# Performance work log

Measured on AMD Instinct MI355X. Metric: run time of the kernel, lower is better.

The kernel has to match this reference:

```python
import jax, jax.numpy as jnp
import numpy as np

B, N, C = 4, 4096, 512
K = 683  # ceil(N / ratio=6.0)
TAU = 1.0
W_OCC, W_REP, W_ENT = 1.0, 0.1, 0.01
REP_TOPK, REP_MARGIN = 4, -1.0
NEG = -1e9


def setup_inputs() -> dict:
    key = jax.random.key(0)
    ks = jax.random.split(key, 5)
    s = jax.random.normal(ks[0], (B, N, C), jnp.float32)
    mu = jax.random.normal(ks[1], (B, N, 3), jnp.float32)
    # SPD covariance per residue: L L^T + 0.1 I
    L = jax.random.normal(ks[2], (B, N, 3, 3), jnp.float32) * 0.3
    Sigma = jnp.einsum('bnij,bnkj->bnik', L, L) + 0.1 * jnp.eye(3, dtype=jnp.float32)
    mask = jnp.ones((B, N), jnp.float32)
    W = jax.random.normal(ks[3], (C, C), jnp.float32) / np.sqrt(C).astype(np.float32)
    b = jnp.zeros((C,), jnp.float32)
    slots = jax.random.normal(ks[4], (K, C), jnp.float32) * 0.02
    return {"s": s, "mu": mu, "Sigma": Sigma, "mask": mask, "W": W, "b": b, "slots": slots}


def reference(s, mu, Sigma, mask, W, b, slots):
    Kk = slots.shape[0]
    # A = softmax((Linear(s)) . slots / tau), masked
    s_proj = jnp.einsum('bnc,dc->bnd', s, W) + b            # nn.Linear: x @ W^T + b
    logits = jnp.einsum('bnc,kc->bnk', s_proj, slots) / TAU
    logits = jnp.where((mask < 0.5)[..., None], NEG, logits)
    A = jax.nn.softmax(logits, axis=-1) * mask[..., None]   # [B,N,K]

    denom = jnp.maximum(A.sum(axis=1), 1e-8)                # [B,K]
    s_c = jnp.einsum('bnk,bnc->bkc', A, s) / denom[..., None]

    # moment-matching merge
    w = A / (A.sum(axis=1, keepdims=True) + 1e-8)           # [B,N,K]
    mu_c = jnp.einsum('bnk,bnd->bkd', w, mu)                # [B,K,3]
    intra = jnp.einsum('bnk,bnij->bkij', w, Sigma)          # [B,K,3,3]
    diff = mu[:, :, None, :] - mu_c[:, None, :, :]          # [B,N,K,3]
    inter = jnp.einsum('bnk,bnki,bnkj->bkij', w, diff, diff)
    Sigma_c = intra + inter                                 # [B,K,3,3]

    # occupancy balance loss
    occ = A.sum(axis=1)
    occ = occ / jnp.maximum(occ.sum(axis=-1, keepdims=True), 1e-8)
    loss_occ = jnp.mean((occ - 1.0 / Kk) ** 2)

    # repulsion loss (pairwise Gaussian overlap)
    delta = mu_c[:, :, None, :] - mu_c[:, None, :, :]       # [B,K,K,3]
    sig_sum = Sigma_c[:, :, None] + Sigma_c[:, None, :]     # [B,K,K,3,3]
    inv = jnp.linalg.inv(sig_sum + 1e-6 * jnp.eye(3, dtype=s.dtype))
    dist2 = jnp.einsum('bpqi,bpqij,bpqj->bpq', delta, inv, delta)
    score = -0.5 * dist2
    eye = jnp.eye(Kk, dtype=bool)[None]
    score = jnp.where(eye, NEG, score)
    top = jax.lax.top_k(score, min(REP_TOPK, Kk - 1))[0]
    loss_rep = jnp.mean(jax.nn.relu(top - REP_MARGIN))

    # entropy loss
    Ac = jnp.maximum(A, 1e-8)
    ent = -(Ac * jnp.log(Ac)).sum(axis=-1)                  # [B,N]
    loss_ent = (ent * mask).sum() / jnp.maximum(mask.sum(), 1.0)

    total = W_OCC * loss_occ + W_REP * loss_rep + W_ENT * loss_ent
    return (A, s_c, mu_c, Sigma_c, loss_occ, loss_rep, loss_ent, total)
```

## Files before the change

kernel.cpp:

```cpp
#include <hip/hip_runtime.h>
#include <math.h>

#define B_    4
#define N_    4096
#define C_    512
#define KSLOT 683

using bf16x8 = __attribute__((ext_vector_type(8))) short;
using f32x4  = __attribute__((ext_vector_type(4))) float;

#define OFF_A    0
#define OFF_SC   (B_*N_*KSLOT)
#define OFF_MU   (OFF_SC + B_*KSLOT*C_)
#define OFF_SIG  (OFF_MU + B_*KSLOT*3)
#define OFF_LOSS (OFF_SIG + B_*KSLOT*9)

#define WS_MOM    0
#define WS_INVMAX (WS_MOM + B_*KSLOT*16)
#define WS_OCCTB  (WS_INVMAX + B_*KSLOT)
#define WS_OCCT   (WS_OCCTB + 256)
#define WS_ENTB   (WS_OCCT + 4)
#define WS_MSB    (WS_ENTB + 256)
#define WS_OCCLB  (WS_MSB + 256)
#define WS_REPB   (WS_OCCLB + 256)
#define WS_BS     (WS_REPB + 256)
#define WS_FEND   (WS_BS + 704)

#define US_BASE  (WS_FEND*2)
#define US_SBF   US_BASE
#define US_STF   (US_SBF + B_*N_*C_)
#define US_WSL   (US_STF + B_*C_*N_)
#define US_FT    (US_WSL + 704*C_)
#define US_ATB   (US_FT + B_*16*N_)
#define US_END   (US_ATB + (size_t)B_*768*N_)


__device__ __forceinline__ ushort f2bf(float x) {
  union { float f; unsigned u; } v; v.f = x;
  unsigned r = v.u + 0x7fffu + ((v.u >> 16) & 1u);
  return (ushort)(r >> 16);
}

__device__ __forceinline__ float blockSum256(float v, float* red) {
#pragma unroll
  for (int off = 32; off; off >>= 1) v += __shfl_xor(v, off);
  __syncthreads();
  if ((threadIdx.x & 63) == 0) red[threadIdx.x >> 6] = v;
  __syncthreads();
  return red[0] + red[1] + red[2] + red[3];
}

__device__ __forceinline__ void top4_insert(float v, float& t0, float& t1, float& t2, float& t3) {
  if (v > t3) {
    if (v > t2) {
      t3 = t2;
      if (v > t1) {
        t2 = t1;
        if (v > t0) { t1 = t0; t0 = v; } else t1 = v;
      } else t2 = v;
    } else t3 = v;
  }
}

__global__ __launch_bounds__(256) void prep_all(const float* __restrict__ s,
                                                ushort* __restrict__ sbf,
                                                ushort* __restrict__ stf,
                                                const float* __restrict__ mu,
                                                const float* __restrict__ Sig,
                                                ushort* __restrict__ ftg,
                                                const float* __restrict__ slots,
                                                const float* __restrict__ W,
                                                ushort* __restrict__ wsl,
                                                const float* __restrict__ bvec,
                                                float* __restrict__ bs) {
  __shared__ __align__(16) char PS[16640];
  const int bid = blockIdx.x;
  const int t = threadIdx.x;
  if (bid < 342) {
    float (*SL)[512] = (float(*)[512])PS;
    const int idx = bid;
    const int k0 = (idx % 171) * 4;
    const int c = (idx / 171) * 256 + t;
    for (int id2 = t; id2 < 4 * 512; id2 += 256) {
      int kk = id2 >> 9, d = id2 & 511;
      SL[kk][d] = (k0 + kk < KSLOT) ? slots[(size_t)(k0 + kk) * C_ + d] : 0.f;
    }
    __syncthreads();
    float acc[4];
#pragma unroll
    for (int i = 0; i < 4; ++i) acc[i] = 0.f;
    for (int d0 = 0; d0 < C_; d0 += 8) {
      float wv[8];
#pragma unroll
      for (int j = 0; j < 8; ++j) wv[j] = W[(size_t)(d0 + j) * C_ + c];
#pragma unroll
      for (int j = 0; j < 8; ++j) {
#pragma unroll
        for (int i = 0; i < 4; ++i) acc[i] += SL[i][d0 + j] * wv[j];
      }
    }
#pragma unroll
    for (int i = 0; i < 4; ++i)
      if (k0 + i < KSLOT) wsl[(size_t)(k0 + i) * C_ + c] = f2bf(acc[i]);
  } else if (bid < 513) {
    const int widx = (bid - 342) * 4 + (t >> 6);
    const int lane = t & 63;
    if (widx < KSLOT) {
      const float* srow = slots + (size_t)widx * C_;
      float acc = 0.f;
#pragma unroll
      for (int j = 0; j < 8; ++j) {
        int d = lane + j * 64;
        acc += srow[d] * bvec[d];
      }
#pragma unroll
      for (int off = 32; off; off >>= 1) acc += __shfl_xor(acc, off);
      if (lane == 0) bs[widx] = acc;
    }
  } else if (bid < 577) {
    ushort (*FT)[272] = (ushort(*)[272])PS;
    const int fb = bid - 513;
    const size_t ng = (size_t)fb * 256 + t;
    const float* mp = mu + ng * 3;
    const float* sp = Sig + ng * 9;
    float m0 = mp[0], m1 = mp[1], m2 = mp[2];
    FT[0][t] = 0x3F80;
    FT[1][t] = f2bf(m0); FT[2][t] = f2bf(m1); FT[3][t] = f2bf(m2);
    FT[4][t] = f2bf(m0 * m0); FT[5][t] = f2bf(m0 * m1); FT[6][t] = f2bf(m0 * m2);
    FT[7][t] = f2bf(m1 * m1); FT[8][t] = f2bf(m1 * m2); FT[9][t] = f2bf(m2 * m2);
    FT[10][t] = f2bf(sp[0]); FT[11][t] = f2bf(sp[1]); FT[12][t] = f2bf(sp[2]);
    FT[13][t] = f2bf(sp[4]); FT[14][t] = f2bf(sp[5]); FT[15][t] = f2bf(sp[8]);
    __syncthreads();
    const int b = (int)((fb * 256) >> 12);
    const int n0b = (fb * 256) & (N_ - 1);
    for (int u = t; u < 512; u += 256) {
      int f = u >> 5, off = (u & 31) * 8;
      *(uint4*)(ftg + ((size_t)b * 16 + f) * N_ + n0b + off) = *(uint4*)(&FT[f][off]);
    }
  } else {
    float (*T)[65] = (float(*)[65])PS;
    const int cid = bid - 577;
    const int b = cid >> 9;
    const int rem = cid & 511;
    const int n0 = (rem >> 3) * 64;
    const int c0 = (rem & 7) * 64;
    const int tr = t >> 4;
    const int tc = (t & 15) * 4;
#pragma unroll
    for (int i = 0; i < 4; ++i) {
      const int row = i * 16 + tr;
      float4 v = *(const float4*)(s + ((size_t)(b * N_ + n0 + row)) * C_ + c0 + tc);
      ushort4 u;
      u.x = f2bf(v.x); u.y = f2bf(v.y); u.z = f2bf(v.z); u.w = f2bf(v.w);
      *(ushort4*)(sbf + ((size_t)(b * N_ + n0 + row)) * C_ + c0 + tc) = u;
      T[row][tc + 0] = v.x; T[row][tc + 1] = v.y;
      T[row][tc + 2] = v.z; T[row][tc + 3] = v.w;
    }
    __syncthreads();
#pragma unroll
    for (int i = 0; i < 4; ++i) {
      const int c = i * 16 + tr;
      const int n4 = tc;
      ushort4 o;
      o.x = f2bf(T[n4 + 0][c]); o.y = f2bf(T[n4 + 1][c]);
      o.z = f2bf(T[n4 + 2][c]); o.w = f2bf(T[n4 + 3][c]);
      *(ushort4*)(stf + ((size_t)(b * C_ + c0 + c)) * N_ + n0 + n4) = o;
    }
  }
}

__global__ __launch_bounds__(256) void bs_kernel(const float* __restrict__ slots,
                                                 const float* __restrict__ bvec,
                                                 float* __restrict__ bs) {
  int k = blockIdx.x * 256 + threadIdx.x;
  if (k >= KSLOT) return;
  const float* srow = slots + (size_t)k * C_;
  float acc = 0.f;
  for (int d = 0; d < C_; ++d) acc += srow[d] * bvec[d];
  bs[k] = acc;
}

__device__ __forceinline__ void g1_epilogue(
    f32x4 (&acc)[11], const int rowbase, const int t, const int lane,
    const int rowg, const int colw,
    const float* __restrict__ bs, const float* __restrict__ mask,
    float* __restrict__ Aout, ushort* __restrict__ atb,
    float* __restrict__ entb, float* __restrict__ msb,
    float* Af, float (&red4)[32][4], const int binid) {
  __syncthreads();
  int cols[11]; bool valid[11];
#pragma unroll
  for (int cf = 0; cf < 11; ++cf) {
    cols[cf] = colw * 176 + cf * 16 + (lane & 15);
    valid[cf] = (cols[cf] < KSLOT);
    float bv = valid[cf] ? bs[cols[cf]] : 0.f;
#pragma unroll
    for (int r = 0; r < 4; ++r) acc[cf][r] += bv;
  }
  float m4[4];
#pragma unroll
  for (int r = 0; r < 4; ++r) m4[r] = -3.0e38f;
#pragma unroll
  for (int cf = 0; cf < 11; ++cf)
    if (valid[cf]) {
#pragma unroll
      for (int r = 0; r < 4; ++r) m4[r] = fmaxf(m4[r], acc[cf][r]);
    }
#pragma unroll
  for (int off = 1; off < 16; off <<= 1) {
#pragma unroll
    for (int r = 0; r < 4; ++r) m4[r] = fmaxf(m4[r], __shfl_xor(m4[r], off));
  }
  if ((lane & 15) == 0) {
#pragma unroll
    for (int r = 0; r < 4; ++r) red4[rowg * 16 + (lane >> 4) * 4 + r][colw] = m4[r];
  }
  __syncthreads();
#pragma unroll
  for (int r = 0; r < 4; ++r) {
    int rl = rowg * 16 + (lane >> 4) * 4 + r;
    m4[r] = fmaxf(fmaxf(red4[rl][0], red4[rl][1]), fmaxf(red4[rl][2], red4[rl][3]));
  }
  __syncthreads();
  float s4[4] = {0.f, 0.f, 0.f, 0.f};
#pragma unroll
  for (int cf = 0; cf < 11; ++cf)
    if (valid[cf]) {
#pragma unroll
      for (int r = 0; r < 4; ++r) {
        float e = __expf(acc[cf][r] - m4[r]);
        acc[cf][r] = e;
        s4[r] += e;
      }
    }
#pragma unroll
  for (int off = 1; off < 16; off <<= 1) {
#pragma unroll
    for (int r = 0; r < 4; ++r) s4[r] += __shfl_xor(s4[r], off);
  }
  if ((lane & 15) == 0) {
#pragma unroll
    for (int r = 0; r < 4; ++r) red4[rowg * 16 + (lane >> 4) * 4 + r][colw] = s4[r];
  }
  __syncthreads();
  float inv4[4], mr4[4];
#pragma unroll
  for (int r = 0; r < 4; ++r) {
    int rl = rowg * 16 + (lane >> 4) * 4 + r;
    float S = red4[rl][0] + red4[rl][1] + red4[rl][2] + red4[rl][3];
    inv4[r] = 1.f / S;
    mr4[r] = mask[rowbase + rl];
  }
  __syncthreads();
  float ent4[4] = {0.f, 0.f, 0.f, 0.f};
#pragma unroll
  for (int cf = 0; cf < 11; ++cf)
    if (valid[cf]) {
#pragma unroll
      for (int r = 0; r < 4; ++r) {
        int rl = rowg * 16 + (lane >> 4) * 4 + r;
        float a = acc[cf][r] * inv4[r] * mr4[r];
        Af[rl * KSLOT + cols[cf]] = a;
        float ac = fmaxf(a, 1e-8f);
        ent4[r] -= ac * __logf(ac);
      }
    }
#pragma unroll
  for (int off = 1; off < 16; off <<= 1) {
#pragma unroll
    for (int r = 0; r < 4; ++r) ent4[r] += __shfl_xor(ent4[r], off);
  }
  if ((lane & 15) == 0) {
#pragma unroll
    for (int r = 0; r < 4; ++r) red4[rowg * 16 + (lane >> 4) * 4 + r][colw] = ent4[r];
  }
  __syncthreads();
  if (t < 64) {
    float er = 0.f, ms = 0.f;
    if (t < 32) {
      float e = red4[t][0] + red4[t][1] + red4[t][2] + red4[t][3];
      float m = mask[rowbase + t];
      er = e * m; ms = m;
    }
#pragma unroll
    for (int off = 32; off; off >>= 1) { er += __shfl_xor(er, off); ms += __shfl_xor(ms, off); }
    if (t == 0) {
      atomicAdd(&entb[binid], er);
      atomicAdd(&msb[binid], ms);
    }
  }
  const float4* Af4 = (const float4*)Af;
  float4* Ag4 = (float4*)(Aout + (size_t)rowbase * KSLOT);
  for (int i = t; i < (32 * KSLOT) / 4; i += 512) Ag4[i] = Af4[i];
  {
    const int bb = rowbase >> 12;
    const int n0b = rowbase & (N_ - 1);
    ushort* Atb = atb + ((size_t)bb * 768) * N_ + n0b;
    for (int u = t; u < KSLOT * 4; u += 512) {
      int k = u >> 2, q = u & 3;
      ushort tmp[8];
#pragma unroll
      for (int j = 0; j < 8; ++j) tmp[j] = f2bf(Af[(q * 8 + j) * KSLOT + k]);
      *(uint4*)(Atb + (size_t)k * N_ + q * 8) = *(uint4*)tmp;
    }
  }
}

__global__ __launch_bounds__(512)
__attribute__((amdgpu_waves_per_eu(2, 2)))
void gemm1sm(const ushort* __restrict__ sbf,
             const ushort* __restrict__ wsl,
             const float* __restrict__ bs,
             const float* __restrict__ mask,
             float* __restrict__ Aout,
             ushort* __restrict__ atb,
             float* __restrict__ entb,
             float* __restrict__ msb) {
  __shared__ __align__(16) char SMEM[90112];
  float* Af = (float*)SMEM;
  __shared__ float red4[32][4];
  const int t = threadIdx.x;
  const int lane = t & 63;
  const int w = t >> 6;
  const int rowg = w >> 2;
  const int colw = w & 3;
  const int row0 = blockIdx.x * 64;
  const int r16 = rowg * 16 + (lane & 15);

  const ushort* arow0 = sbf + (size_t)(row0 + r16) * C_ + (lane >> 4) * 8;
  const ushort* arow1 = arow0 + (size_t)32 * C_;
  bf16x8 g0a = *(const bf16x8*)(arow0);
  bf16x8 g0b = *(const bf16x8*)(arow0 + 32);
  bf16x8 g1a = *(const bf16x8*)(arow1);
  bf16x8 g1b = *(const bf16x8*)(arow1 + 32);
  bf16x8 p0a, p0b, p1a, p1b;

  f32x4 acc0[11], acc1[11];
  f32x4 zero = {0.f, 0.f, 0.f, 0.f};
#pragma unroll
  for (int cf = 0; cf < 11; ++cf) { acc0[cf] = zero; acc1[cf] = zero; }

#pragma unroll
  for (int slab = 0; slab < 8; ++slab) {
    if (slab) __syncthreads();
#pragma unroll
    for (int i = 0; i < 11; ++i) {
      int idx = t + i * 512;
      int r = idx >> 3;
      int chs = (idx & 7) ^ (r & 7);
      const ushort* g = wsl + (size_t)r * C_ + slab * 64 + chs * 8;
      char* l = (char*)SMEM + i * 8192 + (t & 448) * 16;
      __builtin_amdgcn_global_load_lds(
          (const __attribute__((address_space(1))) void*)g,
          (__attribute__((address_space(3))) void*)l, 16, 0, 0);
    }
    __syncthreads();
    if (slab < 7) {
      p0a = *(const bf16x8*)(arow0 + (slab + 1) * 64);
      p0b = *(const bf16x8*)(arow0 + (slab + 1) * 64 + 32);
      p1a = *(const bf16x8*)(arow1 + (slab + 1) * 64);
      p1b = *(const bf16x8*)(arow1 + (slab + 1) * 64 + 32);
    }
    {
      const int ach0 = (lane >> 4);
#pragma unroll
      for (int cf = 0; cf < 11; ++cf) {
        int br = colw * 176 + cf * 16 + (lane & 15);
        bf16x8 bf = *(const bf16x8*)(SMEM + br * 128 + ((ach0 * 16) ^ ((br & 7) << 4)));
        acc0[cf] = __builtin_amdgcn_mfma_f32_16x16x32_bf16(g0a, bf, acc0[cf], 0, 0, 0);
        acc1[cf] = __builtin_amdgcn_mfma_f32_16x16x32_bf16(g1a, bf, acc1[cf], 0, 0, 0);
      }
      const int ach1 = 4 + (lane >> 4);
#pragma unroll
      for (int cf = 0; cf < 11; ++cf) {
        int br = colw * 176 + cf * 16 + (lane & 15);
        bf16x8 bf = *(const bf16x8*)(SMEM + br * 128 + ((ach1 * 16) ^ ((br & 7) << 4)));
        acc0[cf] = __builtin_amdgcn_mfma_f32_16x16x32_bf16(g0b, bf, acc0[cf], 0, 0, 0);
        acc1[cf] = __builtin_amdgcn_mfma_f32_16x16x32_bf16(g1b, bf, acc1[cf], 0, 0, 0);
      }
    }
    g0a = p0a; g0b = p0b; g1a = p1a; g1b = p1b;
  }

  g1_epilogue(acc0, row0, t, lane, rowg, colw, bs, mask, Aout, atb, entb, msb,
              Af, red4, (blockIdx.x * 2) & 255);
  g1_epilogue(acc1, row0 + 32, t, lane, rowg, colw, bs, mask, Aout, atb, entb, msb,
              Af, red4, (blockIdx.x * 2 + 1) & 255);
}

#define G2BUFB 18432
__global__ __launch_bounds__(256) void gemm2t(const ushort* __restrict__ atb,
                                              const ushort* __restrict__ stf,
                                              const ushort* __restrict__ ftg,
                                              float* __restrict__ sc,
                                              float* __restrict__ MOM) {
  __shared__ __align__(16) char LB[2 * G2BUFB];
  const int t = threadIdx.x;
  const int lane = t & 63;
  const int w = t >> 6;
  const int wm = w >> 1;
  const int wn = w & 1;
  const int fhw = blockIdx.x;
  const int logical = (fhw & 7) * 44 + (fhw >> 3);
  const int kt = logical % 11;
  const int ct = (logical / 11) & 7;
  const int b  = logical / 88;
  const bool do_mom = (ct == 0);
  const ushort* Ab = atb + ((size_t)b * 768 + kt * 64) * N_;
  const ushort* Sb = stf + ((size_t)b * C_ + ct * 64) * N_;
  const ushort* Fb = ftg + ((size_t)b * 16) * N_;

  f32x4 zero = {0.f, 0.f, 0.f, 0.f};
  f32x4 acc[2][2];
#pragma unroll
  for (int i = 0; i < 2; ++i)
#pragma unroll
    for (int j = 0; j < 2; ++j) acc[i][j] = zero;
  f32x4 accf[2];
#pragma unroll
  for (int i = 0; i < 2; ++i) accf[i] = zero;

#define G2_STAGE(BUFI, NB)                                                   \
  {                                                                          \
    char* AtL = LB + (BUFI) * G2BUFB;                                        \
    char* SsL = AtL + 8192;                                                  \
    char* FtL = AtL + 16384;                                                 \
    _Pragma("unroll")                                                        \
    for (int i = 0; i < 2; ++i) {                                            \
      int idx = t + i * 256;                                                 \
      int r = idx >> 3;                                                      \
      int chs = (idx & 7) ^ (r & 7);                                         \
      const ushort* g = Ab + (size_t)r * N_ + (NB) + chs * 8;                \
      char* l = AtL + i * 4096 + (t & 192) * 16;                             \
      __builtin_amdgcn_global_load_lds(                                      \
          (const __attribute__((address_space(1))) void*)g,                  \
          (__attribute__((address_space(3))) void*)l, 16, 0, 0);             \
    }                                                                        \
    _Pragma("unroll")                                                        \
    for (int i = 0; i < 2; ++i) {                                            \
      int idx = t + i * 256;                                                 \
      int r = idx >> 3;                                                      \
      int chs = (idx & 7) ^ (r & 7);                                         \
      const ushort* g = Sb + (size_t)r * N_ + (NB) + chs * 8;                \
      char* l = SsL + i * 4096 + (t & 192) * 16;                             \
      __builtin_amdgcn_global_load_lds(                                      \
          (const __attribute__((address_space(1))) void*)g,                  \
          (__attribute__((address_space(3))) void*)l, 16, 0, 0);             \
    }                                                                        \
    if (do_mom && t < 128) {                                                 \
      int idx = t;                                                           \
      int r = idx >> 3;                                                      \
      int chs = (idx & 7) ^ (r & 7);                                         \
      const ushort* g = Fb + (size_t)r * N_ + (NB) + chs * 8;                \
      char* l = FtL + (t & 192) * 16;                                        \
      __builtin_amdgcn_global_load_lds(                                      \
          (const __attribute__((address_space(1))) void*)g,                  \
          (__attribute__((address_space(3))) void*)l, 16, 0, 0);             \
    }                                                                        \
  }

  G2_STAGE(0, 0)
  for (int st = 0; st < 64; ++st) {
    const int cur = st & 1;
    __syncthreads();
    if (st < 63) G2_STAGE(cur ^ 1, (st + 1) * 64)
    char* AtL = LB + cur * G2BUFB;
    char* SsL = AtL + 8192;
    char* FtL = AtL + 16384;
#pragma unroll
    for (int ks2 = 0; ks2 < 2; ++ks2) {
      const int ach = ks2 * 4 + (lane >> 4);
      bf16x8 afr[2], bfr[2];
#pragma unroll
      for (int kf = 0; kf < 2; ++kf) {
        int ar = wm * 32 + kf * 16 + (lane & 15);
        afr[kf] = *(const bf16x8*)(AtL + ar * 128 + ((ach * 16) ^ ((ar & 7) << 4)));
      }
#pragma unroll
      for (int cg = 0; cg < 2; ++cg) {
        int br = wn * 32 + cg * 16 + (lane & 15);
        bfr[cg] = *(const bf16x8*)(SsL + br * 128 + ((ach * 16) ^ ((br & 7) << 4)));
      }
#pragma unroll
      for (int kf = 0; kf < 2; ++kf)
#pragma unroll
        for (int cg = 0; cg < 2; ++cg)
          acc[kf][cg] = __builtin_amdgcn_mfma_f32_16x16x32_bf16(afr[kf], bfr[cg], acc[kf][cg], 0, 0, 0);
      if (do_mom && wn == 0) {
        int fr = lane & 15;
        bf16x8 ffr = *(const bf16x8*)(FtL + fr * 128 + ((ach * 16) ^ ((fr & 7) << 4)));
#pragma unroll
        for (int kf = 0; kf < 2; ++kf)
          accf[kf] = __builtin_amdgcn_mfma_f32_16x16x32_bf16(afr[kf], ffr, accf[kf], 0, 0, 0);
      }
    }
  }
#undef G2_STAGE

#pragma unroll
  for (int kf = 0; kf < 2; ++kf) {
#pragma unroll
    for (int r = 0; r < 4; ++r) {
      int k = kt * 64 + wm * 32 + kf * 16 + (lane >> 4) * 4 + r;
      if (k >= KSLOT) continue;
      float* dst = sc + ((size_t)(b * KSLOT + k)) * C_ + ct * 64 + wn * 32;
#pragma unroll
      for (int cg = 0; cg < 2; ++cg)
        dst[cg * 16 + (lane & 15)] = acc[kf][cg][r];
    }
  }
  if (do_mom && wn == 0) {
#pragma unroll
    for (int kf = 0; kf < 2; ++kf) {
#pragma unroll
      for (int r = 0; r < 4; ++r) {
        int k = kt * 64 + wm * 32 + kf * 16 + (lane >> 4) * 4 + r;
        if (k >= KSLOT) continue;
        MOM[((size_t)b * KSLOT + k) * 16 + (lane & 15)] = accf[kf][r];
      }
    }
  }
}

__global__ __launch_bounds__(128) void scale_sc(float* __restrict__ sc,
                                                const float* __restrict__ invmax) {
  const int bk = blockIdx.x;
  const float sv = invmax[bk];
  float4* p = (float4*)(sc + (size_t)bk * C_);
  int t = threadIdx.x;
  float4 v = p[t];
  v.x *= sv; v.y *= sv; v.z *= sv; v.w *= sv;
  p[t] = v;
}

__global__ __launch_bounds__(256) void moments_kernel(const float* __restrict__ Amat,
                                                      const float* __restrict__ mu,
                                                      const float* __restrict__ Sig,
                                                      float* __restrict__ MOM) {
  __shared__ float red[64][17];
  const int b = blockIdx.z;
  const int kx = threadIdx.x & 63;
  const int k = blockIdx.x * 64 + kx;
  const int ng = threadIdx.x >> 6;
  const int n0 = blockIdx.y * 128;
  const bool valid = (k < KSLOT);

  float acc[16];
#pragma unroll
  for (int i = 0; i < 16; ++i) acc[i] = 0.f;

  const float* Abase = Amat + (size_t)b * N_ * KSLOT + k;
  const float* mubase = mu + ((size_t)b * N_) * 3;
  const float* sgbase = Sig + ((size_t)b * N_) * 9;

  for (int j = 0; j < 32; ++j) {
    const int n = n0 + ng + j * 4;
    float a = valid ? Abase[(size_t)n * KSLOT] : 0.f;
    const float* mp = mubase + (size_t)n * 3;
    const float* sp = sgbase + (size_t)n * 9;
    float m0 = mp[0], m1 = mp[1], m2 = mp[2];
    acc[0] += a;
    acc[1] += a * m0; acc[2] += a * m1; acc[3] += a * m2;
    acc[4] += a * m0 * m0; acc[5] += a * m0 * m1; acc[6] += a * m0 * m2;
    acc[7] += a * m1 * m1; acc[8] += a * m1 * m2; acc[9] += a * m2 * m2;
    acc[10] += a * sp[0]; acc[11] += a * sp[1]; acc[12] += a * sp[2];
    acc[13] += a * sp[4]; acc[14] += a * sp[5]; acc[15] += a * sp[8];
  }

  if (ng == 0) {
#pragma unroll
    for (int i = 0; i < 16; ++i) red[kx][i] = acc[i];
  }
  __syncthreads();
  if (ng == 1) {
#pragma unroll
    for (int i = 0; i < 16; ++i) red[kx][i] += acc[i];
  }
  __syncthreads();
  if (ng == 2) {
#pragma unroll
    for (int i = 0; i < 16; ++i) red[kx][i] += acc[i];
  }
  __syncthreads();
  if (ng == 3) {
#pragma unroll
    for (int i = 0; i < 16; ++i) red[kx][i] += acc[i];
  }
  __syncthreads();
  if (ng == 0 && valid) {
    float* dst = MOM + ((size_t)b * KSLOT + k) * 16;
#pragma unroll
    for (int i = 0; i < 16; ++i) atomicAdd(&dst[i], red[kx][i]);
  }
}

__global__ __launch_bounds__(256) void finalize_bk(const float* __restrict__ MOM,
                                                   float* __restrict__ muc,
                                                   float* __restrict__ sigc,
                                                   float* __restrict__ invmax,
                                                   float* __restrict__ occtb) {
  int bk = blockIdx.x * 256 + threadIdx.x;
  if (bk >= B_ * KSLOT) return;
  int b = bk / KSLOT;
  const float* T = MOM + (size_t)bk * 16;
  float den = T[0];
  float inv_eps = 1.f / (den + 1e-8f);
  float inv_mx = 1.f / fmaxf(den, 1e-8f);
  float mc0 = T[1] * inv_eps, mc1 = T[2] * inv_eps, mc2 = T[3] * inv_eps;
  float M0 = den * inv_eps;
  float cf = 2.f - M0;
  float S00 = (T[10] + T[4]) * inv_eps - cf * mc0 * mc0;
  float S01 = (T[11] + T[5]) * inv_eps - cf * mc0 * mc1;
  float S02 = (T[12] + T[6]) * inv_eps - cf * mc0 * mc2;
  float S11 = (T[13] + T[7]) * inv_eps - cf * mc1 * mc1;
  float S12 = (T[14] + T[8]) * inv_eps - cf * mc1 * mc2;
  float S22 = (T[15] + T[9]) * inv_eps - cf * mc2 * mc2;
  muc[(size_t)bk * 3 + 0] = mc0;
  muc[(size_t)bk * 3 + 1] = mc1;
  muc[(size_t)bk * 3 + 2] = mc2;
  float* sg = sigc + (size_t)bk * 9;
  sg[0] = S00; sg[1] = S01; sg[2] = S02;
  sg[3] = S01; sg[4] = S11; sg[5] = S12;
  sg[6] = S02; sg[7] = S12; sg[8] = S22;
  invmax[bk] = inv_mx;
  atomicAdd(&occtb[b * 64 + (threadIdx.x & 63)], den);
}

__global__ __launch_bounds__(256) void occ_loss_kernel(const float* __restrict__ MOM,
                                                       const float* __restrict__ occtb,
                                                       float* __restrict__ occlb) {
  __shared__ float red[4];
  __shared__ float occT[4];
  int tid = threadIdx.x;
  {
    float v = occtb[tid];
#pragma unroll
    for (int off = 32; off; off >>= 1) v += __shfl_xor(v, off);
    if ((tid & 63) == 0) occT[tid >> 6] = v;
  }
  __syncthreads();
  int bk = blockIdx.x * 256 + tid;
  float d2 = 0.f;
  if (bk < B_ * KSLOT) {
    int b = bk / KSLOT;
    float den = MOM[(size_t)bk * 16];
    float occ = den / fmaxf(occT[b], 1e-8f);
    float d = occ - (1.f / (float)KSLOT);
    d2 = d * d;
  }
  float ssum = blockSum256(d2, red);
  if (tid == 0) occlb[blockIdx.x] = ssum;
}

__global__ __launch_bounds__(256) void repulsion_kernel2(const float* __restrict__ muc,
                                                         const float* __restrict__ sigc,
                                                         float* __restrict__ repb) {
  __shared__ float L[KSLOT * 13];
  const int b = blockIdx.y;
  const int t = threadIdx.x;
  const float* mb = muc + (size_t)b * KSLOT * 3;
  const float* sb = sigc + (size_t)b * KSLOT * 9;
  for (int idx = t; idx < KSLOT * 3; idx += 256) {
    int r = idx / 3, c = idx - r * 3;
    L[r * 13 + c] = mb[idx];
  }
  for (int idx = t; idx < KSLOT * 9; idx += 256) {
    int r = idx / 9, c = idx - r * 9;
    L[r * 13 + 3 + c] = sb[idx];
  }
  __syncthreads();
  const int w = t >> 6, lane = t & 63;
  const int p = blockIdx.x * 4 + w;
  if (p >= KSLOT) return;
  const float* Lp = L + p * 13;
  const float mp0 = Lp[0], mp1 = Lp[1], mp2 = Lp[2];
  const float pa = Lp[3], pb = Lp[4], pc = Lp[5], pd = Lp[7], pe = Lp[8], pf = Lp[11];
  float t0 = -3e38f, t1 = -3e38f, t2 = -3e38f, t3 = -3e38f;
  for (int q = lane; q < KSLOT; q += 64) {
    if (q == p) continue;
    const float* Lq = L + q * 13;
    float d0 = mp0 - Lq[0];
    float d1 = mp1 - Lq[1];
    float d2 = mp2 - Lq[2];
    float a  = pa + Lq[3] + 1e-6f;
    float bb = pb + Lq[4];
    float cc = pc + Lq[5];
    float d  = pd + Lq[7] + 1e-6f;
    float e  = pe + Lq[8];
    float f  = pf + Lq[11] + 1e-6f;
    float C00 = d * f - e * e;
    float C01 = cc * e - bb * f;
    float C02 = bb * e - cc * d;
    float C11 = a * f - cc * cc;
    float C12 = bb * cc - a * e;
    float C22 = a * d - bb * bb;
    float det = a * C00 + bb * C01 + cc * C02;
    float dist2 = (C00 * d0 * d0 + C11 * d1 * d1 + C22 * d2 * d2 +
                   2.f * (C01 * d0 * d1 + C02 * d0 * d2 + C12 * d1 * d2)) / det;
    top4_insert(-0.5f * dist2, t0, t1, t2, t3);
  }
#pragma unroll
  for (int off = 1; off < 64; off <<= 1) {
    float u0 = __shfl_xor(t0, off);
    float u1 = __shfl_xor(t1, off);
    float u2 = __shfl_xor(t2, off);
    float u3 = __shfl_xor(t3, off);
    top4_insert(u0, t0, t1, t2, t3);
    top4_insert(u1, t0, t1, t2, t3);
    top4_insert(u2, t0, t1, t2, t3);
    top4_insert(u3, t0, t1, t2, t3);
  }
  if (lane == 0) {
    float s = fmaxf(t0 + 1.f, 0.f) + fmaxf(t1 + 1.f, 0.f) +
              fmaxf(t2 + 1.f, 0.f) + fmaxf(t3 + 1.f, 0.f);
    atomicAdd(&repb[(b * KSLOT + p) & 255], s);
  }
}

__global__ __launch_bounds__(256) void final_scalars(const float* __restrict__ entb,
                                                     const float* __restrict__ msb,
                                                     const float* __restrict__ occlb,
                                                     const float* __restrict__ repb,
                                                     float* __restrict__ out) {
  __shared__ float red[4];
  int tid = threadIdx.x;
  float e = blockSum256(entb[tid], red);
  float ms = blockSum256(msb[tid], red);
  float oc = blockSum256(occlb[tid], red);
  float rp = blockSum256(repb[tid], red);
  if (tid == 0) {
    float loss_ent = e / fmaxf(ms, 1.f);
    float loss_occ = oc / (float)(B_ * KSLOT);
    float loss_rep = rp / (float)(B_ * KSLOT * 4);
    out[0] = loss_occ;
    out[1] = loss_rep;
    out[2] = loss_ent;
    out[3] = 1.0f * loss_occ + 0.1f * loss_rep + 0.01f * loss_ent;
  }
}


__global__ __launch_bounds__(256) void wslots_kernel(const float* __restrict__ slots,
                                                     const float* __restrict__ W,
                                                     float* __restrict__ Wsl) {
  int k = blockIdx.x;
  int c = blockIdx.y * 256 + threadIdx.x;
  const float* srow = slots + (size_t)k * C_;
  float acc = 0.f;
  for (int d = 0; d < C_; d += 4) {
    acc += srow[d] * W[(size_t)d * C_ + c];
    acc += srow[d + 1] * W[(size_t)(d + 1) * C_ + c];
    acc += srow[d + 2] * W[(size_t)(d + 2) * C_ + c];
    acc += srow[d + 3] * W[(size_t)(d + 3) * C_ + c];
  }
  Wsl[(size_t)k * C_ + c] = acc;
}

__global__ __launch_bounds__(256) void softmax_rows(float* __restrict__ Amat,
                                                    const float* __restrict__ mask,
                                                    float* __restrict__ entb,
                                                    float* __restrict__ msb) {
  __shared__ float red[4];
  const int row = blockIdx.x;
  const int tid = threadIdx.x;
  float* rowp = Amat + (size_t)row * KSLOT;
  const float m = mask[row];
  const bool msk = (m < 0.5f);
  float v[3];
#pragma unroll
  for (int i = 0; i < 3; ++i) {
    int k = tid + i * 256;
    if (k < KSLOT) {
      float l = rowp[k];
      v[i] = msk ? -1e9f : l;
    } else v[i] = -3.0e38f;
  }
  float lmax = fmaxf(fmaxf(v[0], v[1]), v[2]);
#pragma unroll
  for (int off = 32; off; off >>= 1) lmax = fmaxf(lmax, __shfl_xor(lmax, off));
  __syncthreads();
  if ((tid & 63) == 0) red[tid >> 6] = lmax;
  __syncthreads();
  lmax = fmaxf(fmaxf(red[0], red[1]), fmaxf(red[2], red[3]));
  float lsum = 0.f;
#pragma unroll
  for (int i = 0; i < 3; ++i) {
    int k = tid + i * 256;
    float e = (k < KSLOT) ? expf(v[i] - lmax) : 0.f;
    v[i] = e;
    lsum += e;
  }
  lsum = blockSum256(lsum, red);
  float inv = 1.f / lsum;
  float ent = 0.f;
#pragma unroll
  for (int i = 0; i < 3; ++i) {
    int k = tid + i * 256;
    if (k < KSLOT) {
      float a = v[i] * inv * m;
      rowp[k] = a;
      float ac = fmaxf(a, 1e-8f);
      ent -= ac * logf(ac);
    }
  }
  ent = blockSum256(ent, red);
  if (tid == 0) {
    int bin = blockIdx.x & 255;
    atomicAdd(&entb[bin], ent * m);
    atomicAdd(&msb[bin], m);
  }
}

__global__ __launch_bounds__(256) void gemm_nt(const float* __restrict__ Am,
                                               const float* __restrict__ Bm,
                                               const float* __restrict__ bias,
                                               float* __restrict__ Cm,
                                               int M, int Nout, int Kd,
                                               int lda, int ldb, int ldc) {
  __shared__ float As[16][132];
  __shared__ float Bs[16][132];
  const int tid = threadIdx.x;
  const int tx = tid & 15, ty = tid >> 4;
  const int m0 = blockIdx.x * 128, n0 = blockIdx.y * 128;
  float acc[8][8];
#pragma unroll
  for (int i = 0; i < 8; ++i)
#pragma unroll
    for (int j = 0; j < 8; ++j) acc[i][j] = 0.f;
  const int r = tid >> 1, hc = (tid & 1) * 8;
  for (int k0 = 0; k0 < Kd; k0 += 16) {
    float va[8], vb[8];
    int gm = m0 + r;
    if (gm < M) {
      const float* p = Am + (size_t)gm * lda + k0 + hc;
      *(float4*)(va) = *(const float4*)(p);
      *(float4*)(va + 4) = *(const float4*)(p + 4);
    } else {
#pragma unroll
      for (int i = 0; i < 8; ++i) va[i] = 0.f;
    }
    int gn = n0 + r;
    if (gn < Nout) {
      const float* p = Bm + (size_t)gn * ldb + k0 + hc;
      *(float4*)(vb) = *(const float4*)(p);
      *(float4*)(vb + 4) = *(const float4*)(p + 4);
    } else {
#pragma unroll
      for (int i = 0; i < 8; ++i) vb[i] = 0.f;
    }
#pragma unroll
    for (int i = 0; i < 8; ++i) As[hc + i][r] = va[i];
#pragma unroll
    for (int i = 0; i < 8; ++i) Bs[hc + i][r] = vb[i];
    __syncthreads();
#pragma unroll
    for (int kk = 0; kk < 16; ++kk) {
      float a[8], bb[8];
      *(float4*)(a) = *(const float4*)&As[kk][ty * 8];
      *(float4*)(a + 4) = *(const float4*)&As[kk][ty * 8 + 4];
      *(float4*)(bb) = *(const float4*)&Bs[kk][tx * 8];
      *(float4*)(bb + 4) = *(const float4*)&Bs[kk][tx * 8 + 4];
#pragma unroll
      for (int i = 0; i < 8; ++i)
#pragma unroll
        for (int j = 0; j < 8; ++j) acc[i][j] += a[i] * bb[j];
    }
    __syncthreads();
  }
#pragma unroll
  for (int i = 0; i < 8; ++i) {
    int gm = m0 + ty * 8 + i;
    if (gm >= M) continue;
    float* crow = Cm + (size_t)gm * ldc;
#pragma unroll
    for (int j = 0; j < 8; ++j) {
      int gn = n0 + tx * 8 + j;
      if (gn < Nout) crow[gn] = acc[i][j] + bias[gn];
    }
  }
}

__global__ __launch_bounds__(256) void gemm_tn(const float* __restrict__ Aall,
                                               const float* __restrict__ Ball,
                                               const float* __restrict__ scale,
                                               float* __restrict__ Call) {
  const int b = blockIdx.z;
  const float* Am = Aall + (size_t)b * N_ * KSLOT;
  const float* Bv = Ball + (size_t)b * N_ * C_;
  float* Cm = Call + (size_t)b * KSLOT * C_;
  const float* sc = scale + (size_t)b * KSLOT;
  __shared__ float As[16][132];
  __shared__ float Bs[16][68];
  const int tid = threadIdx.x;
  const int tx = tid & 15, ty = tid >> 4;
  const int m0 = blockIdx.x * 128, n0 = blockIdx.y * 64;
  float acc[8][4];
#pragma unroll
  for (int i = 0; i < 8; ++i)
#pragma unroll
    for (int j = 0; j < 4; ++j) acc[i][j] = 0.f;
  const int rr = tid >> 4;
  const int mq = tid & 15;
  const int cq = (tid & 15) * 4;
  for (int r0 = 0; r0 < N_; r0 += 16) {
#pragma unroll
    for (int i = 0; i < 8; ++i) {
      int mm = mq + 16 * i;
      int gm = m0 + mm;
      As[rr][mm] = (gm < KSLOT) ? Am[(size_t)(r0 + rr) * KSLOT + gm] : 0.f;
    }
    *(float4*)&Bs[rr][cq] = *(const float4*)(Bv + (size_t)(r0 + rr) * C_ + n0 + cq);
    __syncthreads();
#pragma unroll
    for (int kk = 0; kk < 16; ++kk) {
      float a[8], bb[4];
      *(float4*)(a) = *(const float4*)&As[kk][ty * 8];
      *(float4*)(a + 4) = *(const float4*)&As[kk][ty * 8 + 4];
      *(float4*)(bb) = *(const float4*)&Bs[kk][tx * 4];
#pragma unroll
      for (int i = 0; i < 8; ++i)
#pragma unroll
        for (int j = 0; j < 4; ++j) acc[i][j] += a[i] * bb[j];
    }
    __syncthreads();
  }
#pragma unroll
  for (int i = 0; i < 8; ++i) {
    int gm = m0 + ty * 8 + i;
    if (gm < KSLOT) {
      float s = sc[gm];
      float4 v;
      v.x = acc[i][0] * s; v.y = acc[i][1] * s; v.z = acc[i][2] * s; v.w = acc[i][3] * s;
      *(float4*)(Cm + (size_t)gm * C_ + n0 + tx * 4) = v;
    }
  }
}

extern "C" void kernel_launch(void* const* d_in, const int* in_sizes, int n_in,
                              void* d_out, int out_size, void* d_ws, size_t ws_size,
                              hipStream_t stream) {
  const float* s     = (const float*)d_in[0];
  const float* mu    = (const float*)d_in[1];
  const float* Sig   = (const float*)d_in[2];
  const float* mask  = (const float*)d_in[3];
  const float* W     = (const float*)d_in[4];
  const float* bvec  = (const float*)d_in[5];
  const float* slots = (const float*)d_in[6];
  float* out = (float*)d_out;
  float* ws  = (float*)d_ws;

  float* Amat = out + OFF_A;
  const bool fast = (ws_size >= (size_t)US_END * 2 + 64);

  (void)hipMemsetAsync(ws, 0, WS_FEND * sizeof(float), stream);

  if (fast) {
    ushort* usw = (ushort*)ws;
    ushort* sbf = usw + US_SBF;
    ushort* stf = usw + US_STF;
    ushort* wsl = usw + US_WSL;
    ushort* ftg = usw + US_FT;
    ushort* atb = usw + US_ATB;

    prep_all<<<dim3(2625), 256, 0, stream>>>(
        s, sbf, stf, mu, Sig, ftg, slots, W, wsl, bvec, ws + WS_BS);

    gemm1sm<<<dim3(B_ * N_ / 64), 512, 0, stream>>>(
        sbf, wsl, ws + WS_BS, mask, Amat, atb, ws + WS_ENTB, ws + WS_MSB);

    gemm2t<<<dim3(352), 256, 0, stream>>>(
        atb, stf, ftg, out + OFF_SC, ws + WS_MOM);

    finalize_bk<<<dim3((B_ * KSLOT + 255) / 256), 256, 0, stream>>>(
        ws + WS_MOM, out + OFF_MU, out + OFF_SIG, ws + WS_INVMAX, ws + WS_OCCTB);

    occ_loss_kernel<<<dim3((B_ * KSLOT + 255) / 256), 256, 0, stream>>>(
        ws + WS_MOM, ws + WS_OCCTB, ws + WS_OCCLB);

    scale_sc<<<dim3(B_ * KSLOT), 128, 0, stream>>>(out + OFF_SC, ws + WS_INVMAX);

    repulsion_kernel2<<<dim3((KSLOT + 3) / 4, B_), 256, 0, stream>>>(
        out + OFF_MU, out + OFF_SIG, ws + WS_REPB);

    final_scalars<<<dim3(1), 256, 0, stream>>>(
        ws + WS_ENTB, ws + WS_MSB, ws + WS_OCCLB, ws + WS_REPB, out + OFF_LOSS);
  } else {
    float* Wsl = out + OFF_SC;

    bs_kernel<<<dim3(3), 256, 0, stream>>>(slots, bvec, ws + WS_BS);
    wslots_kernel<<<dim3(KSLOT, 2), 256, 0, stream>>>(slots, W, Wsl);
    gemm_nt<<<dim3((B_ * N_) / 128, (KSLOT + 127) / 128), 256, 0, stream>>>(
        s, Wsl, ws + WS_BS, Amat, B_ * N_, KSLOT, C_, C_, C_, KSLOT);
    softmax_rows<<<dim3(B_ * N_), 256, 0, stream>>>(Amat, mask, ws + WS_ENTB, ws + WS_MSB);
    moments_kernel<<<dim3(11, N_ / 128, B_), 256, 0, stream>>>(
        Amat, mu, Sig, ws + WS_MOM);
    finalize_bk<<<dim3((B_ * KSLOT + 255) / 256), 256, 0, stream>>>(
        ws + WS_MOM, out + OFF_MU, out + OFF_SIG, ws + WS_INVMAX, ws + WS_OCCTB);
    occ_loss_kernel<<<dim3((B_ * KSLOT + 255) / 256), 256, 0, stream>>>(
        ws + WS_MOM, ws + WS_OCCTB, ws + WS_OCCLB);
    gemm_tn<<<dim3((KSLOT + 127) / 128, C_ / 64, B_), 256, 0, stream>>>(
        Amat, s, ws + WS_INVMAX, out + OFF_SC);
    repulsion_kernel2<<<dim3((KSLOT + 3) / 4, B_), 256, 0, stream>>>(
        out + OFF_MU, out + OFF_SIG, ws + WS_REPB);
    final_scalars<<<dim3(1), 256, 0, stream>>>(
        ws + WS_ENTB, ws + WS_MSB, ws + WS_OCCLB, ws + WS_REPB, out + OFF_LOSS);
  }
}
```

Baseline: 163.6 us.

## Halve gemm1 K-slab, shrink LDS and stage softmax tile in bf16

The first GEMM kernel now streams the slot-weight operand in 32-wide K slabs over 16 iterations instead of 64-wide slabs over 8, which cuts its LDS buffer from about 88 KB to 48 KB. The forced waves-per-EU attribute is dropped so more blocks or waves could be resident. The epilogue stages the softmax tile in LDS as bf16 rather than fp32, halving the staging footprint and removing a conversion in the transpose store. The costs are twice as many barriers and load rounds in the main loop, and the float A output is now rebuilt from bf16-rounded values, so it loses precision.

Result: no change. 164.2 us (+0.4%).

```diff
diff --git a/kernel.cpp b/kernel.cpp
--- a/kernel.cpp
+++ b/kernel.cpp
@@ -39,6 +39,11 @@
   union { float f; unsigned u; } v; v.f = x;
   unsigned r = v.u + 0x7fffu + ((v.u >> 16) & 1u);
   return (ushort)(r >> 16);
+}
+
+__device__ __forceinline__ float bf2f(ushort x) {
+  union { unsigned u; float f; } v; v.u = ((unsigned)x) << 16;
+  return v.f;
 }
 
 __device__ __forceinline__ float blockSum256(float v, float* red) {
@@ -186,7 +191,7 @@
     const float* __restrict__ bs, const float* __restrict__ mask,
     float* __restrict__ Aout, ushort* __restrict__ atb,
     float* __restrict__ entb, float* __restrict__ msb,
-    float* Af, float (&red4)[32][4], const int binid) {
+    ushort* Af, float (&red4)[32][4], const int binid) {
   __syncthreads();
   int cols[11]; bool valid[11];
 #pragma unroll
@@ -260,7 +265,7 @@
       for (int r = 0; r < 4; ++r) {
         int rl = rowg * 16 + (lane >> 4) * 4 + r;
         float a = acc[cf][r] * inv4[r] * mr4[r];
-        Af[rl * KSLOT + cols[cf]] = a;
+        Af[rl * KSLOT + cols[cf]] = f2bf(a);
         float ac = fmaxf(a, 1e-8f);
         ent4[r] -= ac * __logf(ac);
       }
@@ -289,9 +294,13 @@
       atomicAdd(&msb[binid], ms);
     }
   }
-  const float4* Af4 = (const float4*)Af;
-  float4* Ag4 = (float4*)(Aout + (size_t)rowbase * KSLOT);
-  for (int i = t; i < (32 * KSLOT) / 4; i += 512) Ag4[i] = Af4[i];
+  float* Ag = Aout + (size_t)rowbase * KSLOT;
+  for (int i = t; i < (32 * KSLOT) / 4; i += 512) {
+    ushort4 u4 = *(const ushort4*)(Af + i * 4);
+    float4 v;
+    v.x = bf2f(u4.x); v.y = bf2f(u4.y); v.z = bf2f(u4.z); v.w = bf2f(u4.w);
+    *(float4*)(Ag + i * 4) = v;
+  }
   {
     const int bb = rowbase >> 12;
     const int n0b = rowbase & (N_ - 1);
@@ -300,14 +309,13 @@
       int k = u >> 2, q = u & 3;
       ushort tmp[8];
 #pragma unroll
-      for (int j = 0; j < 8; ++j) tmp[j] = f2bf(Af[(q * 8 + j) * KSLOT + k]);
+      for (int j = 0; j < 8; ++j) tmp[j] = Af[(q * 8 + j) * KSLOT + k];
       *(uint4*)(Atb + (size_t)k * N_ + q * 8) = *(uint4*)tmp;
     }
   }
 }
 
 __global__ __launch_bounds__(512)
-__attribute__((amdgpu_waves_per_eu(2, 2)))
 void gemm1sm(const ushort* __restrict__ sbf,
              const ushort* __restrict__ wsl,
              const float* __restrict__ bs,
@@ -316,8 +324,7 @@
              ushort* __restrict__ atb,
              float* __restrict__ entb,
              float* __restrict__ msb) {
-  __shared__ __align__(16) char SMEM[90112];
-  float* Af = (float*)SMEM;
+  __shared__ __align__(16) char SMEM[49152];
   __shared__ float red4[32][4];
   const int t = threadIdx.x;
   const int lane = t & 63;
@@ -329,59 +336,46 @@
 
   const ushort* arow0 = sbf + (size_t)(row0 + r16) * C_ + (lane >> 4) * 8;
   const ushort* arow1 = arow0 + (size_t)32 * C_;
-  bf16x8 g0a = *(const bf16x8*)(arow0);
-  bf16x8 g0b = *(const bf16x8*)(arow0 + 32);
-  bf16x8 g1a = *(const bf16x8*)(arow1);
-  bf16x8 g1b = *(const bf16x8*)(arow1 + 32);
-  bf16x8 p0a, p0b, p1a, p1b;
+  bf16x8 g0 = *(const bf16x8*)(arow0);
+  bf16x8 g1 = *(const bf16x8*)(arow1);
+  bf16x8 p0, p1;
 
   f32x4 acc0[11], acc1[11];
   f32x4 zero = {0.f, 0.f, 0.f, 0.f};
 #pragma unroll
   for (int cf = 0; cf < 11; ++cf) { acc0[cf] = zero; acc1[cf] = zero; }
 
-#pragma unroll
-  for (int slab = 0; slab < 8; ++slab) {
+  const int ach = (lane >> 4);
+#pragma unroll
+  for (int slab = 0; slab < 16; ++slab) {
     if (slab) __syncthreads();
 #pragma unroll
-    for (int i = 0; i < 11; ++i) {
+    for (int i = 0; i < 6; ++i) {
       int idx = t + i * 512;
-      int r = idx >> 3;
-      int chs = (idx & 7) ^ (r & 7);
-      const ushort* g = wsl + (size_t)r * C_ + slab * 64 + chs * 8;
-      char* l = (char*)SMEM + i * 8192 + (t & 448) * 16;
+      int r = idx >> 2;
+      int chs = (idx & 3) ^ (r & 3);
+      const ushort* g = wsl + (size_t)r * C_ + slab * 32 + chs * 8;
+      char* l = (char*)SMEM + (t & 448) * 16 + i * 8192;
       __builtin_amdgcn_global_load_lds(
           (const __attribute__((address_space(1))) void*)g,
           (__attribute__((address_space(3))) void*)l, 16, 0, 0);
     }
     __syncthreads();
-    if (slab < 7) {
-      p0a = *(const bf16x8*)(arow0 + (slab + 1) * 64);
-      p0b = *(const bf16x8*)(arow0 + (slab + 1) * 64 + 32);
-      p1a = *(const bf16x8*)(arow1 + (slab + 1) * 64);
-      p1b = *(const bf16x8*)(arow1 + (slab + 1) * 64 + 32);
-    }
-    {
-      const int ach0 = (lane >> 4);
-#pragma unroll
-      for (int cf = 0; cf < 11; ++cf) {
-        int br = colw * 176 + cf * 16 + (lane & 15);
-        bf16x8 bf = *(const bf16x8*)(SMEM + br * 128 + ((ach0 * 16) ^ ((br & 7) << 4)));
-        acc0[cf] = __builtin_amdgcn_mfma_f32_16x16x32_bf16(g0a, bf, acc0[cf], 0, 0, 0);
-        acc1[cf] = __builtin_amdgcn_mfma_f32_16x16x32_bf16(g1a, bf, acc1[cf], 0, 0, 0);
-      }
-      const int ach1 = 4 + (lane >> 4);
-#pragma unroll
-      for (int cf = 0; cf < 11; ++cf) {
-        int br = colw * 176 + cf * 16 + (lane & 15);
-        bf16x8 bf = *(const bf16x8*)(SMEM + br * 128 + ((ach1 * 16) ^ ((br & 7) << 4)));
-        acc0[cf] = __builtin_amdgcn_mfma_f32_16x16x32_bf16(g0b, bf, acc0[cf], 0, 0, 0);
-        acc1[cf] = __builtin_amdgcn_mfma_f32_16x16x32_bf16(g1b, bf, acc1[cf], 0, 0, 0);
-      }
-    }
-    g0a = p0a; g0b = p0b; g1a = p1a; g1b = p1b;
-  }
-
+    if (slab < 15) {
+      p0 = *(const bf16x8*)(arow0 + (slab + 1) * 32);
+      p1 = *(const bf16x8*)(arow1 + (slab + 1) * 32);
+    }
+#pragma unroll
+    for (int cf = 0; cf < 11; ++cf) {
+      int br = colw * 176 + cf * 16 + (lane & 15);
+      bf16x8 bf = *(const bf16x8*)(SMEM + br * 64 + ((ach * 16) ^ ((br & 3) << 4)));
+      acc0[cf] = __builtin_amdgcn_mfma_f32_16x16x32_bf16(g0, bf, acc0[cf], 0, 0, 0);
+      acc1[cf] = __builtin_amdgcn_mfma_f32_16x16x32_bf16(g1, bf, acc1[cf], 0, 0, 0);
+    }
+    g0 = p0; g1 = p1;
+  }
+
+  ushort* Af = (ushort*)SMEM;
   g1_epilogue(acc0, row0, t, lane, rowg, colw, bs, mask, Aout, atb, entb, msb,
               Af, red4, (blockIdx.x * 2) & 255);
   g1_epilogue(acc1, row0 + 32, t, lane, rowg, colw, bs, mask, Aout, atb, entb, msb,
@@ -452,7 +446,7 @@
       int r = idx >> 3;                                                      \
       int chs = (idx & 7) ^ (r & 7);                                         \
       const ushort* g = Fb + (size_t)r * N_ + (NB) + chs * 8;                \
-      char* l = FtL + (t & 192) * 16;                                        \
+      char* l = FtL + (t & 192) * 16;                                       \
       __builtin_amdgcn_global_load_lds(                                      \
           (const __attribute__((address_space(1))) void*)g,                  \
           (__attribute__((address_space(3))) void*)l, 16, 0, 0);             \
```
